# Optimization experiments

Hardware: AMD Instinct MI355X
Metric: run time of the kernel (lower is better)

## Reference

```python
import jax, jax.numpy as jnp
import numpy as np

# Model config (mirrors Kitnet after initialization):
INPUT_SIZE = 1000
M = 10                 # max_autoencoder_size -> features per cluster
N_CLUSTERS = INPUT_SIZE // M   # 100 tiny autoencoders
HIDDEN_RATIO = 0.5
H_SMALL = max(3, int(M * HIDDEN_RATIO))          # 5
H_META = max(3, int(N_CLUSTERS * HIDDEN_RATIO))  # 50
BATCH = 65536


def setup_inputs() -> dict:
    key = jax.random.key(0)
    ks = jax.random.split(key, 8)
    x = jax.random.normal(ks[0], (BATCH, INPUT_SIZE), dtype=jnp.float32)
    # cluster feature indices: a random permutation of features split into
    # N_CLUSTERS groups of M (equal-size clusters, faithful to gather pattern)
    perm = jax.random.permutation(ks[1], INPUT_SIZE)
    feat_idx = perm.reshape(N_CLUSTERS, M).astype(jnp.int32)
    # per-cluster AE params (PyTorch Linear default init ~ U(-1/sqrt(fan_in),..))
    def lin_init(k, shape, fan_in):
        b = 1.0 / np.sqrt(fan_in)
        return jax.random.uniform(k, shape, minval=-b, maxval=b, dtype=jnp.float32)
    W_enc = lin_init(ks[2], (N_CLUSTERS, M, H_SMALL), M)
    b_enc = lin_init(ks[3], (N_CLUSTERS, H_SMALL), M)
    W_dec = lin_init(ks[4], (N_CLUSTERS, H_SMALL, M), H_SMALL)
    b_dec = lin_init(ks[5], (N_CLUSTERS, M), H_SMALL)
    # meta autoencoder params
    We1 = lin_init(ks[6], (N_CLUSTERS, H_META), N_CLUSTERS)
    k7, k8, k9 = jax.random.split(ks[7], 3)
    be1 = lin_init(k7, (H_META,), N_CLUSTERS)
    Wd1 = lin_init(k8, (H_META, N_CLUSTERS), H_META)
    bd1 = lin_init(k9, (N_CLUSTERS,), H_META)
    return {"x": x, "feat_idx": feat_idx,
            "W_enc": W_enc, "b_enc": b_enc, "W_dec": W_dec, "b_dec": b_dec,
            "We1": We1, "be1": be1, "Wd1": Wd1, "bd1": bd1}


def reference(x, feat_idx, W_enc, b_enc, W_dec, b_dec, We1, be1, Wd1, bd1):
    # gather per-cluster features: [B, C, M]
    xg = x[:, feat_idx]
    # encoder: relu(xg @ W_enc + b_enc) -> [B, C, H]
    h = jax.nn.relu(jnp.einsum('bcm,cmh->bch', xg, W_enc) + b_enc)
    # decoder -> [B, C, M]
    rec = jnp.einsum('bch,chm->bcm', h, W_dec) + b_dec
    # per-cluster RMSE -> [B, C]
    err = jnp.sqrt(jnp.mean((xg - rec) ** 2, axis=-1))
    # meta autoencoder over reconstruction errors
    hm = jax.nn.relu(err @ We1 + be1)
    err_rec = hm @ Wd1 + bd1
    final_error = jnp.sqrt(jnp.mean((err - err_rec) ** 2, axis=-1))
    return jax.nn.sigmoid(final_error)
```

## Files before the change

kernel.cpp:

```cpp
#include <hip/hip_runtime.h>
#include <stdint.h>

typedef _Float16 h2 __attribute__((ext_vector_type(2)));

#define N_CLUSTERS 100
#define M 10
#define HS 5
#define HM 50
#define GROUP 64
#define TILES 4
#define NWAVE 16
#define XPITCH_B 2004

#define O_WE1T 0
#define O_WD1T 5200
#define O_HMT  15600
#define O_PART 22000
#define O_LWE  128256
#define O_LWD  138656
#define O_ERR  150656
#define LDS_TOTAL 163456

__device__ __forceinline__ float fdot2(uint32_t a, uint32_t b, float c) {
    return __builtin_amdgcn_fdot2(__builtin_bit_cast(h2, a),
                                  __builtin_bit_cast(h2, b), c, false);
}
__device__ __forceinline__ uint32_t pk2(float a, float b) {
    return __builtin_bit_cast(uint32_t, __builtin_amdgcn_cvt_pkrtz(a, b));
}
__device__ __forceinline__ float h2f(unsigned short u) {
    return (float)__builtin_bit_cast(_Float16, u);
}

__global__ void __launch_bounds__(1024) kitnet_kernel(
    const float* __restrict__ x,
    const int*   __restrict__ fi,
    const float* __restrict__ W_enc, const float* __restrict__ b_enc,
    const float* __restrict__ W_dec, const float* __restrict__ b_dec,
    const float* __restrict__ We1,   const float* __restrict__ be1,
    const float* __restrict__ Wd1,   const float* __restrict__ bd1,
    float* __restrict__ out)
{
    extern __shared__ char smem[];
    const int tid  = threadIdx.x;
    const int lane = tid & 63;
    const int w    = __builtin_amdgcn_readfirstlane(tid >> 6);

    uint32_t* lweU = (uint32_t*)(smem + O_LWE);
    uint32_t* lwdU = (uint32_t*)(smem + O_LWD);
    unsigned short* errL = (unsigned short*)(smem + O_ERR);

    auto load_x = [&](float4 (&vb)[16], int row0) {
        const float4* xr = (const float4*)(x + (size_t)row0 * 1000);
        #pragma unroll
        for (int k = 0; k < 16; ++k) {
            int i = tid + (k << 10);
            if (i < 16000) vb[k] = xr[i];
        }
    };
    auto write_x = [&](float4 (&vb)[16]) {
        #pragma unroll
        for (int k = 0; k < 16; ++k) {
            int i = tid + (k << 10);
            if (i < 16000) {
                int row = i / 250;
                int c4  = i - row * 250;
                uint32_t* p = (uint32_t*)(smem + row * XPITCH_B + c4 * 8);
                p[0] = pk2(vb[k].x, vb[k].y);
                p[1] = pk2(vb[k].z, vb[k].w);
            }
        }
    };

    const int rowbase = blockIdx.x * (GROUP * TILES);

    float4 vbuf[16];
    load_x(vbuf, rowbase);
    for (int i = tid; i < 2500; i += 1024) {
        int c = i / 25, r = i - c * 25;
        int k = r / 5, pp = r - k * 5;
        lweU[c * 26 + r] = pk2(W_enc[c * 50 + (2 * pp) * 5 + k],
                               W_enc[c * 50 + (2 * pp + 1) * 5 + k]);
    }
    for (int i = tid; i < 3000; i += 1024) {
        int c = i / 30, r = i - c * 30;
        int m = r / 3, q = r - m * 3;
        float lo = W_dec[c * 50 + (2 * q) * 10 + m];
        float hi = (q == 2) ? 0.f : W_dec[c * 50 + (2 * q + 1) * 10 + m];
        lwdU[c * 30 + r] = pk2(lo, hi);
    }
    write_x(vbuf);
    __syncthreads();

    const unsigned short* myrow = (const unsigned short*)(smem + lane * XPITCH_B);
    auto do_cluster = [&](int c) {
        int cols[M];
        #pragma unroll
        for (int m = 0; m < M; ++m) cols[m] = fi[c * 10 + m];
        uint32_t xpk[5];
        #pragma unroll
        for (int p = 0; p < 5; ++p)
            xpk[p] = (uint32_t)myrow[cols[2 * p]] |
                     ((uint32_t)myrow[cols[2 * p + 1]] << 16);
        const uint2* eW = (const uint2*)(lweU + c * 26);
        uint32_t wreg[25];
        #pragma unroll
        for (int q = 0; q < 12; ++q) { uint2 t = eW[q]; wreg[2*q] = t.x; wreg[2*q+1] = t.y; }
        wreg[24] = (lweU + c * 26)[24];
        float h[HS];
        #pragma unroll
        for (int k = 0; k < HS; ++k) h[k] = b_enc[c * 5 + k];
        #pragma unroll
        for (int k = 0; k < HS; ++k) {
            #pragma unroll
            for (int p = 0; p < 5; ++p)
                h[k] = fdot2(xpk[p], wreg[k * 5 + p], h[k]);
        }
        uint32_t hp[3];
        hp[0] = pk2(fmaxf(h[0], 0.f), fmaxf(h[1], 0.f));
        hp[1] = pk2(fmaxf(h[2], 0.f), fmaxf(h[3], 0.f));
        hp[2] = pk2(fmaxf(h[4], 0.f), 0.f);
        const uint2* dW = (const uint2*)(lwdU + c * 30);
        uint32_t dreg[30];
        #pragma unroll
        for (int q = 0; q < 15; ++q) { uint2 t = dW[q]; dreg[2*q] = t.x; dreg[2*q+1] = t.y; }
        float acc = 0.f;
        #pragma unroll
        for (int m = 0; m < M; ++m) {
            float r = b_dec[c * 10 + m];
            r = fdot2(hp[0], dreg[m * 3 + 0], r);
            r = fdot2(hp[1], dreg[m * 3 + 1], r);
            r = fdot2(hp[2], dreg[m * 3 + 2], r);
            h2 xv = __builtin_bit_cast(h2, xpk[m >> 1]);
            float xf = (float)((m & 1) ? xv.y : xv.x);
            float d = xf - r;
            acc = __builtin_fmaf(d, d, acc);
        }
        _Float16 ev = (_Float16)__builtin_sqrtf(acc * 0.1f);
        errL[lane * 100 + c] = __builtin_bit_cast(unsigned short, ev);
    };

    uint32_t* we1U = (uint32_t*)(smem + O_WE1T);
    uint32_t* wd1U = (uint32_t*)(smem + O_WD1T);
    uint32_t* hmp  = (uint32_t*)(smem + O_HMT);
    float*    part = (float*)(smem + O_PART);
    const uint2* e2 = (const uint2*)(errL + lane * 100);
    auto do_pair = [&](int p) {
        const int j0 = 2 * p;
        float a0 = be1[j0], a1 = be1[j0 + 1];
        const uint2* w0 = (const uint2*)(we1U + j0 * 26);
        const uint2* w1 = (const uint2*)(we1U + (j0 + 1) * 26);
        #pragma unroll
        for (int ch = 0; ch < 12; ++ch) {
            uint2 e = e2[ch]; uint2 wa = w0[ch]; uint2 wb = w1[ch];
            a0 = fdot2(e.x, wa.x, a0); a0 = fdot2(e.y, wa.y, a0);
            a1 = fdot2(e.x, wb.x, a1); a1 = fdot2(e.y, wb.y, a1);
        }
        uint32_t et = ((const uint32_t*)e2)[24];
        a0 = fdot2(et, (we1U + j0 * 26)[24], a0);
        a1 = fdot2(et, (we1U + (j0 + 1) * 26)[24], a1);
        hmp[p * 64 + lane] = pk2(fmaxf(a0, 0.f), fmaxf(a1, 0.f));
    };

    #pragma unroll 1
    for (int t = 0; t < TILES; ++t) {
        const int b0t = rowbase + t * GROUP;

        #pragma unroll 2
        for (int u = 0; u < 6; ++u) do_cluster(w + 16 * u);
        if (w < 4) do_cluster(w + 96);
        __syncthreads();

        if (t + 1 < TILES) load_x(vbuf, b0t + GROUP);

        for (int i = tid; i < 1250; i += 1024) {
            int j = i / 25, cp = i - j * 25;
            we1U[j * 26 + cp] = pk2(We1[(2 * cp) * 50 + j], We1[(2 * cp + 1) * 50 + j]);
        }
        for (int i = tid; i < 2500; i += 1024) {
            int c = i / 25, jp = i - c * 25;
            wd1U[c * 26 + jp] = pk2(Wd1[(2 * jp) * 100 + c], Wd1[(2 * jp + 1) * 100 + c]);
        }
        __syncthreads();

        do_pair(w);
        if (w < 9) do_pair(w + 16);
        __syncthreads();

        uint32_t hmreg[25];
        #pragma unroll
        for (int p = 0; p < 25; ++p) hmreg[p] = hmp[p * 64 + lane];
        float facc = 0.f;
        auto do_dec = [&](int c) {
            float er = h2f(errL[lane * 100 + c]);
            float r = bd1[c];
            const uint2* wr = (const uint2*)(wd1U + c * 26);
            #pragma unroll
            for (int q = 0; q < 12; ++q) {
                uint2 tt = wr[q];
                r = fdot2(hmreg[2 * q], tt.x, r);
                r = fdot2(hmreg[2 * q + 1], tt.y, r);
            }
            r = fdot2(hmreg[24], (wd1U + c * 26)[24], r);
            float d = er - r;
            facc = __builtin_fmaf(d, d, facc);
        };
        #pragma unroll 2
        for (int u = 0; u < 6; ++u) do_dec(w + 16 * u);
        if (w < 4) do_dec(w + 96);
        part[w * 64 + lane] = facc;
        __syncthreads();

        if (tid < 64) {
            float s = 0.f;
            #pragma unroll
            for (int i = 0; i < NWAVE; ++i) s += part[i * 64 + tid];
            float fe = __builtin_sqrtf(s * 0.01f);
            out[b0t + tid] = 1.f / (1.f + __expf(-fe));
        }
        __syncthreads();

        if (t + 1 < TILES) write_x(vbuf);
        __syncthreads();
    }
}

extern "C" void kernel_launch(void* const* d_in, const int* in_sizes, int n_in,
                              void* d_out, int out_size, void* d_ws, size_t ws_size,
                              hipStream_t stream) {
    const float* x     = (const float*)d_in[0];
    const int*   fi    = (const int*)  d_in[1];
    const float* W_enc = (const float*)d_in[2];
    const float* b_enc = (const float*)d_in[3];
    const float* W_dec = (const float*)d_in[4];
    const float* b_dec = (const float*)d_in[5];
    const float* We1   = (const float*)d_in[6];
    const float* be1   = (const float*)d_in[7];
    const float* Wd1   = (const float*)d_in[8];
    const float* bd1   = (const float*)d_in[9];
    float* out = (float*)d_out;

    (void)hipFuncSetAttribute((const void*)kitnet_kernel,
                              hipFuncAttributeMaxDynamicSharedMemorySize, LDS_TOTAL);
    kitnet_kernel<<<65536 / (GROUP * TILES), 1024, LDS_TOTAL, stream>>>(
        x, fi, W_enc, b_enc, W_dec, b_dec, We1, be1, Wd1, bd1, out);
}
```

Measured before the change: 433.8 us.

## Precompute packed weights in a prep kernel and drop LDS weight staging

Adds a small prep kernel that packs the per-cluster, meta-encoder and meta-decoder weights, biases and feature indices into an fp16-packed workspace layout. The main kernel then reads them directly from global memory with wave-uniform addresses, so they can go through scalar loads, instead of rebuilding LDS copies in every block and every tile. It also moves the next-tile x prefetch earlier, writes x into LDS right after the cluster phase, and removes two barriers per tile. The cost is an extra kernel launch and reliance on the scalar/L2 cache path for the weights.

```diff
diff --git a/kernel.cpp b/kernel.cpp
--- a/kernel.cpp
+++ b/kernel.cpp
@@ -12,14 +12,14 @@
 #define NWAVE 16
 #define XPITCH_B 2004
 
-#define O_WE1T 0
-#define O_WD1T 5200
-#define O_HMT  15600
-#define O_PART 22000
-#define O_LWE  128256
-#define O_LWD  138656
-#define O_ERR  150656
-#define LDS_TOTAL 163456
+#define O_ERR  128256
+#define O_HMT  141056
+#define O_PART 147456
+#define LDS_TOTAL 151552
+
+#define WS_META  8000
+#define WS_DEC   9300
+#define WS_U32   11900
 
 __device__ __forceinline__ float fdot2(uint32_t a, uint32_t b, float c) {
     return __builtin_amdgcn_fdot2(__builtin_bit_cast(h2, a),
@@ -31,14 +31,57 @@
 __device__ __forceinline__ float h2f(unsigned short u) {
     return (float)__builtin_bit_cast(_Float16, u);
 }
-
-__global__ void __launch_bounds__(1024) kitnet_kernel(
-    const float* __restrict__ x,
+__device__ __forceinline__ float asf(uint32_t u) {
+    return __builtin_bit_cast(float, u);
+}
+
+__global__ void __launch_bounds__(256) prep_kernel(
     const int*   __restrict__ fi,
     const float* __restrict__ W_enc, const float* __restrict__ b_enc,
     const float* __restrict__ W_dec, const float* __restrict__ b_dec,
     const float* __restrict__ We1,   const float* __restrict__ be1,
     const float* __restrict__ Wd1,   const float* __restrict__ bd1,
+    uint32_t* __restrict__ ws)
+{
+    int idx = blockIdx.x * 256 + threadIdx.x;
+    if (idx < 8000) {
+        int c = idx / 80, r = idx - c * 80;
+        uint32_t v;
+        if (r < 10) v = (uint32_t)fi[c * 10 + r];
+        else if (r < 35) {
+            int q = r - 10; int k = q / 5, p = q - k * 5;
+            v = pk2(W_enc[c * 50 + (2 * p) * 5 + k],
+                    W_enc[c * 50 + (2 * p + 1) * 5 + k]);
+        } else if (r < 40) v = __builtin_bit_cast(uint32_t, b_enc[c * 5 + (r - 35)]);
+        else if (r < 70) {
+            int q = r - 40; int m = q / 3, qq = q - m * 3;
+            float lo = W_dec[c * 50 + (2 * qq) * 10 + m];
+            float hi = (qq == 2) ? 0.f : W_dec[c * 50 + (2 * qq + 1) * 10 + m];
+            v = pk2(lo, hi);
+        } else v = __builtin_bit_cast(uint32_t, b_dec[c * 10 + (r - 70)]);
+        ws[idx] = v;
+    } else if (idx < WS_META + 25 * 52) {
+        int t = idx - WS_META; int p = t / 52, r = t - p * 52;
+        int j0 = 2 * p;
+        uint32_t v;
+        if (r < 25)      v = pk2(We1[(2 * r) * 50 + j0], We1[(2 * r + 1) * 50 + j0]);
+        else if (r < 50) { int cp = r - 25;
+                           v = pk2(We1[(2 * cp) * 50 + j0 + 1], We1[(2 * cp + 1) * 50 + j0 + 1]); }
+        else if (r == 50) v = __builtin_bit_cast(uint32_t, be1[j0]);
+        else              v = __builtin_bit_cast(uint32_t, be1[j0 + 1]);
+        ws[idx] = v;
+    } else if (idx < WS_U32) {
+        int t = idx - WS_DEC; int c = t / 26, r = t - c * 26;
+        uint32_t v;
+        if (r < 25) v = pk2(Wd1[(2 * r) * 100 + c], Wd1[(2 * r + 1) * 100 + c]);
+        else        v = __builtin_bit_cast(uint32_t, bd1[c]);
+        ws[idx] = v;
+    }
+}
+
+__global__ void __launch_bounds__(1024, 4) kitnet_kernel(
+    const float* __restrict__ x,
+    const uint32_t* __restrict__ ws,
     float* __restrict__ out)
 {
     extern __shared__ char smem[];
@@ -46,9 +89,9 @@
     const int lane = tid & 63;
     const int w    = __builtin_amdgcn_readfirstlane(tid >> 6);
 
-    uint32_t* lweU = (uint32_t*)(smem + O_LWE);
-    uint32_t* lwdU = (uint32_t*)(smem + O_LWD);
     unsigned short* errL = (unsigned short*)(smem + O_ERR);
+    uint32_t* hmp  = (uint32_t*)(smem + O_HMT);
+    float*    part = (float*)(smem + O_PART);
 
     auto load_x = [&](float4 (&vb)[16], int row0) {
         const float4* xr = (const float4*)(x + (size_t)row0 * 1000);
@@ -76,61 +119,37 @@
 
     float4 vbuf[16];
     load_x(vbuf, rowbase);
-    for (int i = tid; i < 2500; i += 1024) {
-        int c = i / 25, r = i - c * 25;
-        int k = r / 5, pp = r - k * 5;
-        lweU[c * 26 + r] = pk2(W_enc[c * 50 + (2 * pp) * 5 + k],
-                               W_enc[c * 50 + (2 * pp + 1) * 5 + k]);
-    }
-    for (int i = tid; i < 3000; i += 1024) {
-        int c = i / 30, r = i - c * 30;
-        int m = r / 3, q = r - m * 3;
-        float lo = W_dec[c * 50 + (2 * q) * 10 + m];
-        float hi = (q == 2) ? 0.f : W_dec[c * 50 + (2 * q + 1) * 10 + m];
-        lwdU[c * 30 + r] = pk2(lo, hi);
-    }
     write_x(vbuf);
     __syncthreads();
 
     const unsigned short* myrow = (const unsigned short*)(smem + lane * XPITCH_B);
     auto do_cluster = [&](int c) {
-        int cols[M];
-        #pragma unroll
-        for (int m = 0; m < M; ++m) cols[m] = fi[c * 10 + m];
+        const uint32_t* rec = ws + c * 80;
         uint32_t xpk[5];
         #pragma unroll
-        for (int p = 0; p < 5; ++p)
-            xpk[p] = (uint32_t)myrow[cols[2 * p]] |
-                     ((uint32_t)myrow[cols[2 * p + 1]] << 16);
-        const uint2* eW = (const uint2*)(lweU + c * 26);
-        uint32_t wreg[25];
-        #pragma unroll
-        for (int q = 0; q < 12; ++q) { uint2 t = eW[q]; wreg[2*q] = t.x; wreg[2*q+1] = t.y; }
-        wreg[24] = (lweU + c * 26)[24];
+        for (int p = 0; p < 5; ++p) {
+            int c0 = (int)rec[2 * p], c1 = (int)rec[2 * p + 1];
+            xpk[p] = (uint32_t)myrow[c0] | ((uint32_t)myrow[c1] << 16);
+        }
         float h[HS];
         #pragma unroll
-        for (int k = 0; k < HS; ++k) h[k] = b_enc[c * 5 + k];
+        for (int k = 0; k < HS; ++k) h[k] = asf(rec[35 + k]);
         #pragma unroll
         for (int k = 0; k < HS; ++k) {
             #pragma unroll
             for (int p = 0; p < 5; ++p)
-                h[k] = fdot2(xpk[p], wreg[k * 5 + p], h[k]);
-        }
-        uint32_t hp[3];
-        hp[0] = pk2(fmaxf(h[0], 0.f), fmaxf(h[1], 0.f));
-        hp[1] = pk2(fmaxf(h[2], 0.f), fmaxf(h[3], 0.f));
-        hp[2] = pk2(fmaxf(h[4], 0.f), 0.f);
-        const uint2* dW = (const uint2*)(lwdU + c * 30);
-        uint32_t dreg[30];
-        #pragma unroll
-        for (int q = 0; q < 15; ++q) { uint2 t = dW[q]; dreg[2*q] = t.x; dreg[2*q+1] = t.y; }
+                h[k] = fdot2(xpk[p], rec[10 + k * 5 + p], h[k]);
+        }
+        uint32_t hp0 = pk2(fmaxf(h[0], 0.f), fmaxf(h[1], 0.f));
+        uint32_t hp1 = pk2(fmaxf(h[2], 0.f), fmaxf(h[3], 0.f));
+        uint32_t hp2 = pk2(fmaxf(h[4], 0.f), 0.f);
         float acc = 0.f;
         #pragma unroll
         for (int m = 0; m < M; ++m) {
-            float r = b_dec[c * 10 + m];
-            r = fdot2(hp[0], dreg[m * 3 + 0], r);
-            r = fdot2(hp[1], dreg[m * 3 + 1], r);
-            r = fdot2(hp[2], dreg[m * 3 + 2], r);
+            float r = asf(rec[70 + m]);
+            r = fdot2(hp0, rec[40 + m * 3 + 0], r);
+            r = fdot2(hp1, rec[40 + m * 3 + 1], r);
+            r = fdot2(hp2, rec[40 + m * 3 + 2], r);
             h2 xv = __builtin_bit_cast(h2, xpk[m >> 1]);
             float xf = (float)((m & 1) ? xv.y : xv.x);
             float d = xf - r;
@@ -140,25 +159,19 @@
         errL[lane * 100 + c] = __builtin_bit_cast(unsigned short, ev);
     };
 
-    uint32_t* we1U = (uint32_t*)(smem + O_WE1T);
-    uint32_t* wd1U = (uint32_t*)(smem + O_WD1T);
-    uint32_t* hmp  = (uint32_t*)(smem + O_HMT);
-    float*    part = (float*)(smem + O_PART);
     const uint2* e2 = (const uint2*)(errL + lane * 100);
     auto do_pair = [&](int p) {
-        const int j0 = 2 * p;
-        float a0 = be1[j0], a1 = be1[j0 + 1];
-        const uint2* w0 = (const uint2*)(we1U + j0 * 26);
-        const uint2* w1 = (const uint2*)(we1U + (j0 + 1) * 26);
+        const uint32_t* mr = ws + WS_META + p * 52;
+        float a0 = asf(mr[50]), a1 = asf(mr[51]);
         #pragma unroll
         for (int ch = 0; ch < 12; ++ch) {
-            uint2 e = e2[ch]; uint2 wa = w0[ch]; uint2 wb = w1[ch];
-            a0 = fdot2(e.x, wa.x, a0); a0 = fdot2(e.y, wa.y, a0);
-            a1 = fdot2(e.x, wb.x, a1); a1 = fdot2(e.y, wb.y, a1);
+            uint2 e = e2[ch];
+            a0 = fdot2(e.x, mr[2 * ch], a0);      a0 = fdot2(e.y, mr[2 * ch + 1], a0);
+            a1 = fdot2(e.x, mr[25 + 2 * ch], a1); a1 = fdot2(e.y, mr[25 + 2 * ch + 1], a1);
         }
         uint32_t et = ((const uint32_t*)e2)[24];
-        a0 = fdot2(et, (we1U + j0 * 26)[24], a0);
-        a1 = fdot2(et, (we1U + (j0 + 1) * 26)[24], a1);
+        a0 = fdot2(et, mr[24], a0);
+        a1 = fdot2(et, mr[49], a1);
         hmp[p * 64 + lane] = pk2(fmaxf(a0, 0.f), fmaxf(a1, 0.f));
     };
 
@@ -166,22 +179,14 @@
     for (int t = 0; t < TILES; ++t) {
         const int b0t = rowbase + t * GROUP;
 
-        #pragma unroll 2
+        if (t + 1 < TILES) load_x(vbuf, b0t + GROUP);
+
+        #pragma unroll 1
         for (int u = 0; u < 6; ++u) do_cluster(w + 16 * u);
         if (w < 4) do_cluster(w + 96);
         __syncthreads();
 
-        if (t + 1 < TILES) load_x(vbuf, b0t + GROUP);
-
-        for (int i = tid; i < 1250; i += 1024) {
-            int j = i / 25, cp = i - j * 25;
-            we1U[j * 26 + cp] = pk2(We1[(2 * cp) * 50 + j], We1[(2 * cp + 1) * 50 + j]);
-        }
-        for (int i = tid; i < 2500; i += 1024) {
-            int c = i / 25, jp = i - c * 25;
-            wd1U[c * 26 + jp] = pk2(Wd1[(2 * jp) * 100 + c], Wd1[(2 * jp + 1) * 100 + c]);
-        }
-        __syncthreads();
+        if (t + 1 < TILES) write_x(vbuf);
 
         do_pair(w);
         if (w < 9) do_pair(w + 16);
@@ -192,16 +197,15 @@
         for (int p = 0; p < 25; ++p) hmreg[p] = hmp[p * 64 + lane];
         float facc = 0.f;
         auto do_dec = [&](int c) {
+            const uint32_t* dr = ws + WS_DEC + c * 26;
             float er = h2f(errL[lane * 100 + c]);
-            float r = bd1[c];
-            const uint2* wr = (const uint2*)(wd1U + c * 26);
+            float r = asf(dr[25]);
             #pragma unroll
             for (int q = 0; q < 12; ++q) {
-                uint2 tt = wr[q];
-                r = fdot2(hmreg[2 * q], tt.x, r);
-                r = fdot2(hmreg[2 * q + 1], tt.y, r);
+                r = fdot2(hmreg[2 * q], dr[2 * q], r);
+                r = fdot2(hmreg[2 * q + 1], dr[2 * q + 1], r);
             }
-            r = fdot2(hmreg[24], (wd1U + c * 26)[24], r);
+            r = fdot2(hmreg[24], dr[24], r);
             float d = er - r;
             facc = __builtin_fmaf(d, d, facc);
         };
@@ -218,10 +222,6 @@
             float fe = __builtin_sqrtf(s * 0.01f);
             out[b0t + tid] = 1.f / (1.f + __expf(-fe));
         }
-        __syncthreads();
-
-        if (t + 1 < TILES) write_x(vbuf);
-        __syncthreads();
     }
 }
 
@@ -239,9 +239,13 @@
     const float* Wd1   = (const float*)d_in[8];
     const float* bd1   = (const float*)d_in[9];
     float* out = (float*)d_out;
+    uint32_t* ws = (uint32_t*)d_ws;
+    (void)ws_size;
+
+    prep_kernel<<<(WS_U32 + 255) / 256, 256, 0, stream>>>(
+        fi, W_enc, b_enc, W_dec, b_dec, We1, be1, Wd1, bd1, ws);
 
     (void)hipFuncSetAttribute((const void*)kitnet_kernel,
                               hipFuncAttributeMaxDynamicSharedMemorySize, LDS_TOTAL);
-    kitnet_kernel<<<65536 / (GROUP * TILES), 1024, LDS_TOTAL, stream>>>(
-        x, fi, W_enc, b_enc, W_dec, b_dec, We1, be1, Wd1, bd1, out);
-}
+    kitnet_kernel<<<65536 / (GROUP * TILES), 1024, LDS_TOTAL, stream>>>(x, ws, out);
+}
```

Result: faster. 403.7 us (-7.0%).
